# Kernel tuning notes

Measured on AMD Instinct MI355X. Metric: run time of the kernel, lower is better.

The kernel has to match this reference:

```python
import jax, jax.numpy as jnp
import numpy as np

DIM = 512
HEADS = 8
HEAD_DIM = DIM // HEADS
B, S = 2, 4096


def rope(x):
    # x: [b, s, h, d]
    half = x.shape[-1] // 2
    freqs = 10000.0 ** (-jnp.linspace(0.0, 1.0, half, endpoint=False))  # [half]
    theta = jnp.arange(x.shape[1], dtype=jnp.float32)[None, :, None, None] * freqs[None, None, None, :]
    cos, sin = jnp.cos(theta), jnp.sin(theta)
    rx, ry = x[..., :half], x[..., half:]
    return jnp.concatenate((rx * cos - ry * sin, rx * sin + ry * cos), axis=-1)


def setup_inputs() -> dict:
    key = jax.random.key(0)
    ks = jax.random.split(key, 9)
    sd_in = 1.0 / np.sqrt(DIM)
    sd_o = 1.0 / np.sqrt(DIM)
    return {
        "x": jax.random.normal(ks[0], (B, S, DIM), jnp.float32),
        "wq_k": jax.random.normal(ks[1], (DIM, HEADS, HEAD_DIM), jnp.float32) * sd_in,
        "wq_b": jnp.zeros((HEADS, HEAD_DIM), jnp.float32),
        "wk_k": jax.random.normal(ks[2], (DIM, HEADS, HEAD_DIM), jnp.float32) * sd_in,
        "wk_b": jnp.zeros((HEADS, HEAD_DIM), jnp.float32),
        "wv_k": jax.random.normal(ks[3], (DIM, HEADS, HEAD_DIM), jnp.float32) * sd_in,
        "wv_b": jnp.zeros((HEADS, HEAD_DIM), jnp.float32),
        "wo_k": jax.random.normal(ks[4], (HEADS, HEAD_DIM, DIM), jnp.float32) * sd_o,
        "wo_b": jnp.zeros((DIM,), jnp.float32),
    }


def reference(x, wq_k, wq_b, wk_k, wk_b, wv_k, wv_b, wo_k, wo_b):
    q = rope(jnp.einsum("bsd,dhk->bshk", x, wq_k) + wq_b)
    k = rope(jnp.einsum("bsd,dhk->bshk", x, wk_k) + wk_b)
    v = jnp.einsum("bsd,dhk->bshk", x, wv_k) + wv_b
    scores = jnp.einsum("bqhd,bkhd->bhqk", q, k) / (HEAD_DIM ** 0.5)
    attn = jax.nn.softmax(scores, axis=-1)
    o = jnp.einsum("bhqk,bkhd->bqhd", attn, v)
    return jnp.einsum("bqhd,hdm->bqm", o, wo_k) + wo_b
```

## Files before the change

### kernel.cpp

```cpp
#include <hip/hip_runtime.h>

typedef __bf16 bf16x4 __attribute__((ext_vector_type(4)));
typedef __bf16 bf16x8 __attribute__((ext_vector_type(8)));
typedef float  f32x4  __attribute__((ext_vector_type(4)));

#define MFMA(a, b, c) __builtin_amdgcn_mfma_f32_16x16x32_bf16(a, b, c, 0, 0, 0)

static constexpr int kHeads = 8;
static constexpr int kS     = 4096;

#define CSC 0.18033688011112042f
#define LF  (13.287712379549449f / 32.0f)
#define INV2PI 0.15915494309189535f

__device__ inline float fexp2(float x) {
#if __has_builtin(__builtin_amdgcn_exp2f)
  return __builtin_amdgcn_exp2f(x);
#else
  return __expf(x * 0.6931471805599453f);
#endif
}
__device__ inline float fsin_rev(float rev) {
#if __has_builtin(__builtin_amdgcn_sinf)
  return __builtin_amdgcn_sinf(rev);
#else
  return __sinf(rev * 6.283185307179586f);
#endif
}
__device__ inline float fcos_rev(float rev) {
#if __has_builtin(__builtin_amdgcn_cosf)
  return __builtin_amdgcn_cosf(rev);
#else
  return __cosf(rev * 6.283185307179586f);
#endif
}

__device__ inline int perm32(int d) {
  return (((d >> 2) & 3) << 3) + (((d >> 4) & 1) << 2) + (d & 3);
}

__device__ inline void gl16(const void* src, void* lds) {
  __builtin_amdgcn_global_load_lds(
      (const __attribute__((address_space(1))) unsigned int*)src,
      (__attribute__((address_space(3))) unsigned int*)lds, 16, 0, 0);
}

__global__ __launch_bounds__(256) void wprep(
    const float* __restrict__ w0, const float* __restrict__ w1,
    const float* __restrict__ w2, __bf16* __restrict__ dstb) {
  const int kb32 = blockIdx.x, m = blockIdx.y;
  const float* W = (m == 0) ? w0 : (m == 1) ? w1 : w2;
  bf16x8* dst = (bf16x8*)dstb;
  for (int e = threadIdx.x; e < 2048; e += 256) {
    int lg = e >> 9, col = e & 511;
    bf16x8 v;
    #pragma unroll
    for (int j = 0; j < 8; ++j) {
      int k = kb32 * 32 + 4 * lg + (j & 3) + 16 * (j >> 2);
      v[j] = (__bf16)W[(size_t)k * 512 + col];
    }
    dst[(((size_t)m * 16 + kb32) * 4 + lg) * 512 + col] = v;
  }
}

__global__ __launch_bounds__(256) void qkv(
    const float* __restrict__ x, const __bf16* __restrict__ Wqkvb,
    const float* __restrict__ bq, const float* __restrict__ bk,
    const float* __restrict__ bv,
    __bf16* __restrict__ Qb, __bf16* __restrict__ Kb, __bf16* __restrict__ Vt)
{
  const int tt   = blockIdx.x;
  const int hp   = blockIdx.y;
  const int wave = threadIdx.x >> 6;
  const int lane = threadIdx.x & 63;
  const int l15  = lane & 15;
  const int lg   = lane >> 4;

  const int tok0 = tt * 64 + wave * 16;
  const float* xrow = x + (size_t)(tok0 + l15) * 512;
  const bf16x8* Wf = (const bf16x8*)Wqkvb;

  f32x4 acc[6][4];
  #pragma unroll
  for (int t = 0; t < 6; ++t)
    #pragma unroll
    for (int cb = 0; cb < 4; ++cb) acc[t][cb] = f32x4{0.f, 0.f, 0.f, 0.f};

  for (int kb32 = 0; kb32 < 16; ++kb32) {
    f32x4 xa  = *(const f32x4*)(xrow + kb32 * 32 + 4 * lg);
    f32x4 xb4 = *(const f32x4*)(xrow + kb32 * 32 + 16 + 4 * lg);
    bf16x8 af;
    af[0] = (__bf16)xa.x; af[1] = (__bf16)xa.y; af[2] = (__bf16)xa.z; af[3] = (__bf16)xa.w;
    af[4] = (__bf16)xb4.x; af[5] = (__bf16)xb4.y; af[6] = (__bf16)xb4.z; af[7] = (__bf16)xb4.w;
    #pragma unroll
    for (int t = 0; t < 6; ++t) {
      const int m = t >> 1, hh = t & 1;
      const int colb = (hp * 2 + hh) * 64;
      const bf16x8* wrow = Wf + (((size_t)m * 16 + kb32) * 4 + lg) * 512 + colb + l15;
      #pragma unroll
      for (int cb = 0; cb < 4; ++cb)
        acc[t][cb] = MFMA(af, wrow[cb * 16], acc[t][cb]);
    }
  }

  const float frrev0 = fexp2(-LF * (float)l15) * INV2PI;
  const float frrev1 = fexp2(-LF * (float)(16 + l15)) * INV2PI;
  float snv[4][2], csv[4][2];
  #pragma unroll
  for (int r = 0; r < 4; ++r) {
    float sp = (float)((tok0 + 4 * lg + r) & (kS - 1));
    #pragma unroll
    for (int cb = 0; cb < 2; ++cb) {
      float rev = sp * (cb == 0 ? frrev0 : frrev1);
      rev -= floorf(rev);
      snv[r][cb] = fsin_rev(rev);
      csv[r][cb] = fcos_rev(rev);
    }
  }

  #pragma unroll
  for (int t = 0; t < 6; ++t) {
    const int m = t >> 1, hh = t & 1;
    const int h = hp * 2 + hh;
    const float* bias = (m == 0) ? bq : (m == 1) ? bk : bv;
    #pragma unroll
    for (int cb = 0; cb < 4; ++cb) {
      float bv_ = bias[h * 64 + cb * 16 + l15];
      #pragma unroll
      for (int r = 0; r < 4; ++r) acc[t][cb][r] += bv_;
    }
    if (m < 2) {
      #pragma unroll
      for (int r = 0; r < 4; ++r)
        #pragma unroll
        for (int cb = 0; cb < 2; ++cb) {
          float rx = acc[t][cb][r], ry = acc[t][cb + 2][r];
          acc[t][cb][r]     = rx * csv[r][cb] - ry * snv[r][cb];
          acc[t][cb + 2][r] = rx * snv[r][cb] + ry * csv[r][cb];
        }
      if (m == 0) {
        #pragma unroll
        for (int cb = 0; cb < 4; ++cb)
          #pragma unroll
          for (int r = 0; r < 4; ++r) acc[t][cb][r] *= CSC;
      }
    }
    #pragma unroll
    for (int r = 0; r < 4; ++r) {
      int tok = tok0 + 4 * lg + r;
      int b = tok >> 12, srow = tok & (kS - 1);
      size_t bh = (size_t)(b * kHeads + h);
      #pragma unroll
      for (int cb = 0; cb < 4; ++cb) {
        int d = cb * 16 + l15;
        __bf16 v = (__bf16)acc[t][cb][r];
        if (m < 2) {
          int slot = (d & ~31) + perm32(d & 31);
          if (m == 0) Qb[(bh * kS + srow) * 64 + slot] = v;
          else        Kb[(bh * kS + srow) * 64 + slot] = v;
        } else {
          Vt[((size_t)bh * 64 + d) * kS + (srow & ~31) + perm32(srow & 31)] = v;
        }
      }
    }
  }
}

__global__ __launch_bounds__(512) void attn(
    const __bf16* __restrict__ Qb, const __bf16* __restrict__ Kb,
    const __bf16* __restrict__ Vt, __bf16* __restrict__ Ob)
{
  __shared__ __align__(16) char smem[32768];

  const int id   = blockIdx.x;
  const int bh   = ((id & 7) << 1) | ((id >> 3) & 1);
  const int qt   = id >> 4;
  const int tid  = threadIdx.x;
  const int wave = tid >> 6;
  const int lane = tid & 63;
  const int l15  = lane & 15;
  const int lg   = lane >> 4;

  const __bf16* Qp = Qb + (size_t)bh * kS * 64;
  const char*   Kp = (const char*)(Kb + (size_t)bh * kS * 64);
  const char*   Vp = (const char*)(Vt + (size_t)bh * 64 * kS);

  const int q0 = qt * 128 + wave * 16;

  bf16x8 qf[2];
  #pragma unroll
  for (int dh = 0; dh < 2; ++dh)
    qf[dh] = *(const bf16x8*)(Qp + (size_t)(q0 + l15) * 64 + dh * 32 + 8 * lg);

  const int srow = wave * 8 + (lane >> 3);
  const int ssw  = ((lane & 7) * 16) ^ ((srow & 7) << 4);
  const char* ksrc = Kp + (size_t)srow * 128 + ssw;
  const char* vsrc = Vp + (size_t)srow * 8192 + ssw;
  const int   kdst = wave * 1024;
  const int   vdst = 8192 + wave * 1024;

  const int swz = (l15 & 7) << 4;
  const int ka0 = l15 * 128 + ((16 * lg) ^ swz);
  const int ka1 = l15 * 128 + ((64 + 16 * lg) ^ swz);
  const int va0 = 8192 + ka0;
  const int va1 = 8192 + ka1;

  f32x4 oacc[4];
  #pragma unroll
  for (int db = 0; db < 4; ++db) oacc[db] = f32x4{0.f, 0.f, 0.f, 0.f};
  float lp = 0.f;

  {
    gl16(ksrc, smem + kdst);
    gl16(vsrc, smem + vdst);
    ksrc += 8192; vsrc += 128;
  }

  int buf = 0;
  for (int it = 0; it < kS / 64; ++it) {
    __syncthreads();
    if (it + 1 < kS / 64) {
      char* sb = smem + ((buf ^ 1) << 14);
      gl16(ksrc, sb + kdst);
      gl16(vsrc, sb + vdst);
      ksrc += 8192; vsrc += 128;
    }
    const char* sb = smem + (buf << 14);

    f32x4 sa[4];
    __builtin_amdgcn_s_setprio(1);
    #pragma unroll
    for (int kh = 0; kh < 4; ++kh) {
      sa[kh] = f32x4{0.f, 0.f, 0.f, 0.f};
      bf16x8 kf0 = *(const bf16x8*)(sb + kh * 2048 + ka0);
      bf16x8 kf1 = *(const bf16x8*)(sb + kh * 2048 + ka1);
      sa[kh] = MFMA(kf0, qf[0], sa[kh]);
      sa[kh] = MFMA(kf1, qf[1], sa[kh]);
    }
    __builtin_amdgcn_s_setprio(0);

    bf16x8 pa[2];
    #pragma unroll
    for (int kh = 0; kh < 4; ++kh)
      #pragma unroll
      for (int rr = 0; rr < 4; ++rr) {
        float p = fexp2(sa[kh][rr]);
        lp += p;
        pa[kh >> 1][(kh & 1) * 4 + rr] = (__bf16)p;
      }

    __builtin_amdgcn_s_setprio(1);
    #pragma unroll
    for (int db = 0; db < 4; ++db) {
      bf16x8 vf0 = *(const bf16x8*)(sb + db * 2048 + va0);
      bf16x8 vf1 = *(const bf16x8*)(sb + db * 2048 + va1);
      oacc[db] = MFMA(vf0, pa[0], oacc[db]);
      oacc[db] = MFMA(vf1, pa[1], oacc[db]);
    }
    __builtin_amdgcn_s_setprio(0);
    buf ^= 1;
  }

  float lrun = lp;
  lrun += __shfl_xor(lrun, 16);
  lrun += __shfl_xor(lrun, 32);
  float inv = 1.0f / lrun;

  const int b = bh >> 3, h = bh & 7;
  const int q = q0 + l15;
  #pragma unroll
  for (int db = 0; db < 4; ++db) {
    bf16x4 o4;
    #pragma unroll
    for (int rr = 0; rr < 4; ++rr) o4[rr] = (__bf16)(oacc[db][rr] * inv);
    size_t e = ((size_t)(b * kS + q)) * 512 + h * 64 + (db >> 1) * 32 + 8 * lg + 4 * (db & 1);
    *(bf16x4*)(Ob + e) = o4;
  }
}

__global__ __launch_bounds__(256) void oproj(
    const __bf16* __restrict__ Ob, const __bf16* __restrict__ Wofb,
    const float* __restrict__ wob, float* __restrict__ out)
{
  const int tt   = blockIdx.x;
  const int ct   = blockIdx.y;
  const int wave = threadIdx.x >> 6;
  const int lane = threadIdx.x & 63;
  const int l15  = lane & 15;
  const int lg   = lane >> 4;

  const int tok0 = tt * 64 + wave * 16;
  const int colbase = ct * 64;
  const __bf16* orow = Ob + (size_t)(tok0 + l15) * 512;
  const bf16x8* Wf = (const bf16x8*)Wofb;

  f32x4 acc[4];
  #pragma unroll
  for (int cb = 0; cb < 4; ++cb) acc[cb] = f32x4{0.f, 0.f, 0.f, 0.f};

  for (int kb32 = 0; kb32 < 16; ++kb32) {
    bf16x8 af = *(const bf16x8*)(orow + kb32 * 32 + 8 * lg);
    const bf16x8* wrow = Wf + ((size_t)kb32 * 4 + lg) * 512 + colbase + l15;
    #pragma unroll
    for (int cb = 0; cb < 4; ++cb)
      acc[cb] = MFMA(af, wrow[cb * 16], acc[cb]);
  }

  #pragma unroll
  for (int cb = 0; cb < 4; ++cb) {
    int col = colbase + cb * 16 + l15;
    float bv_ = wob[col];
    #pragma unroll
    for (int r = 0; r < 4; ++r) {
      int tok = tok0 + 4 * lg + r;
      out[(size_t)tok * 512 + col] = acc[cb][r] + bv_;
    }
  }
}

extern "C" void kernel_launch(void* const* d_in, const int* in_sizes, int n_in,
                              void* d_out, int out_size, void* d_ws, size_t ws_size,
                              hipStream_t stream)
{
  const float* x   = (const float*)d_in[0];
  const float* wq  = (const float*)d_in[1];
  const float* bq  = (const float*)d_in[2];
  const float* wk  = (const float*)d_in[3];
  const float* bk  = (const float*)d_in[4];
  const float* wv  = (const float*)d_in[5];
  const float* bv  = (const float*)d_in[6];
  const float* wo  = (const float*)d_in[7];
  const float* wob = (const float*)d_in[8];
  float* out = (float*)d_out;

  const size_t n = (size_t)8192 * 512;
  __bf16* Qb   = (__bf16*)d_ws;
  __bf16* Kb   = Qb + n;
  __bf16* Vt   = Kb + n;
  __bf16* Ob   = Vt + n;
  __bf16* Wqkv = Ob;
  __bf16* Wof  = Qb;

  wprep<<<dim3(16, 3), 256, 0, stream>>>(wq, wk, wv, Wqkv);
  qkv<<<dim3(128, 4), 256, 0, stream>>>(x, Wqkv, bq, bk, bv, Qb, Kb, Vt);
  attn<<<512, 512, 0, stream>>>(Qb, Kb, Vt, Ob);
  wprep<<<dim3(16, 1), 256, 0, stream>>>(wo, wo, wo, Wof);
  oproj<<<dim3(128, 8), 256, 0, stream>>>(Ob, Wof, wob, out);
}
```

Measured before the change: 136.7 us.

## Double attention key tile to 128 and split QKV projection per head

The attention kernel now stages 128 keys per iteration instead of 64, using 64KB of LDS with double buffering. This halves the number of barriers and loop iterations, and each wave issues more MFMAs per sync. The V tile layout changes to 256-byte rows with a new swizzle to match. Separately, the QKV projection launches one block per head instead of per head pair, which halves the accumulator registers and doubles the grid. The cost is that x is loaded and converted twice as often, and the larger LDS footprint may lower attention occupancy.

```diff
diff --git a/kernel.cpp b/kernel.cpp
--- a/kernel.cpp
+++ b/kernel.cpp
@@ -70,7 +70,7 @@
     __bf16* __restrict__ Qb, __bf16* __restrict__ Kb, __bf16* __restrict__ Vt)
 {
   const int tt   = blockIdx.x;
-  const int hp   = blockIdx.y;
+  const int h    = blockIdx.y;
   const int wave = threadIdx.x >> 6;
   const int lane = threadIdx.x & 63;
   const int l15  = lane & 15;
@@ -79,12 +79,13 @@
   const int tok0 = tt * 64 + wave * 16;
   const float* xrow = x + (size_t)(tok0 + l15) * 512;
   const bf16x8* Wf = (const bf16x8*)Wqkvb;
-
-  f32x4 acc[6][4];
-  #pragma unroll
-  for (int t = 0; t < 6; ++t)
-    #pragma unroll
-    for (int cb = 0; cb < 4; ++cb) acc[t][cb] = f32x4{0.f, 0.f, 0.f, 0.f};
+  const int colb = h * 64;
+
+  f32x4 acc[3][4];
+  #pragma unroll
+  for (int m = 0; m < 3; ++m)
+    #pragma unroll
+    for (int cb = 0; cb < 4; ++cb) acc[m][cb] = f32x4{0.f, 0.f, 0.f, 0.f};
 
   for (int kb32 = 0; kb32 < 16; ++kb32) {
     f32x4 xa  = *(const f32x4*)(xrow + kb32 * 32 + 4 * lg);
@@ -93,13 +94,11 @@
     af[0] = (__bf16)xa.x; af[1] = (__bf16)xa.y; af[2] = (__bf16)xa.z; af[3] = (__bf16)xa.w;
     af[4] = (__bf16)xb4.x; af[5] = (__bf16)xb4.y; af[6] = (__bf16)xb4.z; af[7] = (__bf16)xb4.w;
     #pragma unroll
-    for (int t = 0; t < 6; ++t) {
-      const int m = t >> 1, hh = t & 1;
-      const int colb = (hp * 2 + hh) * 64;
+    for (int m = 0; m < 3; ++m) {
       const bf16x8* wrow = Wf + (((size_t)m * 16 + kb32) * 4 + lg) * 512 + colb + l15;
       #pragma unroll
       for (int cb = 0; cb < 4; ++cb)
-        acc[t][cb] = MFMA(af, wrow[cb * 16], acc[t][cb]);
+        acc[m][cb] = MFMA(af, wrow[cb * 16], acc[m][cb]);
     }
   }
 
@@ -119,30 +118,28 @@
   }
 
   #pragma unroll
-  for (int t = 0; t < 6; ++t) {
-    const int m = t >> 1, hh = t & 1;
-    const int h = hp * 2 + hh;
+  for (int m = 0; m < 3; ++m) {
     const float* bias = (m == 0) ? bq : (m == 1) ? bk : bv;
     #pragma unroll
     for (int cb = 0; cb < 4; ++cb) {
-      float bv_ = bias[h * 64 + cb * 16 + l15];
-      #pragma unroll
-      for (int r = 0; r < 4; ++r) acc[t][cb][r] += bv_;
+      float bv_ = bias[colb + cb * 16 + l15];
+      #pragma unroll
+      for (int r = 0; r < 4; ++r) acc[m][cb][r] += bv_;
     }
     if (m < 2) {
       #pragma unroll
       for (int r = 0; r < 4; ++r)
         #pragma unroll
         for (int cb = 0; cb < 2; ++cb) {
-          float rx = acc[t][cb][r], ry = acc[t][cb + 2][r];
-          acc[t][cb][r]     = rx * csv[r][cb] - ry * snv[r][cb];
-          acc[t][cb + 2][r] = rx * snv[r][cb] + ry * csv[r][cb];
+          float rx = acc[m][cb][r], ry = acc[m][cb + 2][r];
+          acc[m][cb][r]     = rx * csv[r][cb] - ry * snv[r][cb];
+          acc[m][cb + 2][r] = rx * snv[r][cb] + ry * csv[r][cb];
         }
       if (m == 0) {
         #pragma unroll
         for (int cb = 0; cb < 4; ++cb)
           #pragma unroll
-          for (int r = 0; r < 4; ++r) acc[t][cb][r] *= CSC;
+          for (int r = 0; r < 4; ++r) acc[m][cb][r] *= CSC;
       }
     }
     #pragma unroll
@@ -153,7 +150,7 @@
       #pragma unroll
       for (int cb = 0; cb < 4; ++cb) {
         int d = cb * 16 + l15;
-        __bf16 v = (__bf16)acc[t][cb][r];
+        __bf16 v = (__bf16)acc[m][cb][r];
         if (m < 2) {
           int slot = (d & ~31) + perm32(d & 31);
           if (m == 0) Qb[(bh * kS + srow) * 64 + slot] = v;
@@ -170,7 +167,7 @@
     const __bf16* __restrict__ Qb, const __bf16* __restrict__ Kb,
     const __bf16* __restrict__ Vt, __bf16* __restrict__ Ob)
 {
-  __shared__ __align__(16) char smem[32768];
+  __shared__ __align__(16) char smem[65536];
 
   const int id   = blockIdx.x;
   const int bh   = ((id & 7) << 1) | ((id >> 3) & 1);
@@ -192,18 +189,22 @@
   for (int dh = 0; dh < 2; ++dh)
     qf[dh] = *(const bf16x8*)(Qp + (size_t)(q0 + l15) * 64 + dh * 32 + 8 * lg);
 
-  const int srow = wave * 8 + (lane >> 3);
-  const int ssw  = ((lane & 7) * 16) ^ ((srow & 7) << 4);
-  const char* ksrc = Kp + (size_t)srow * 128 + ssw;
-  const char* vsrc = Vp + (size_t)srow * 8192 + ssw;
-  const int   kdst = wave * 1024;
-  const int   vdst = 8192 + wave * 1024;
+  const int krow = tid >> 3;
+  const int kssw = ((tid & 7) * 16) ^ ((krow & 7) << 4);
+  const char* ksrc = Kp + (size_t)krow * 128 + kssw;
+  const int vrow = tid >> 4;
+  const int vssw = ((tid & 15) * 16) ^ ((vrow & 7) << 4);
+  const char* vsrc = Vp + (size_t)vrow * 8192 + vssw;
+  const int kdst = wave * 1024;
+  const int vdst = 16384 + wave * 1024;
 
   const int swz = (l15 & 7) << 4;
   const int ka0 = l15 * 128 + ((16 * lg) ^ swz);
   const int ka1 = l15 * 128 + ((64 + 16 * lg) ^ swz);
-  const int va0 = 8192 + ka0;
-  const int va1 = 8192 + ka1;
+  int vko[4];
+  #pragma unroll
+  for (int kv = 0; kv < 4; ++kv)
+    vko[kv] = 16384 + l15 * 256 + ((kv * 64 + 16 * lg) ^ swz);
 
   f32x4 oacc[4];
   #pragma unroll
@@ -211,26 +212,26 @@
   float lp = 0.f;
 
   {
-    gl16(ksrc, smem + kdst);
-    gl16(vsrc, smem + vdst);
-    ksrc += 8192; vsrc += 128;
+    gl16(ksrc, smem + kdst);            gl16(ksrc + 8192, smem + 8192 + kdst);
+    gl16(vsrc, smem + vdst);            gl16(vsrc + 262144, smem + 8192 + vdst);
+    ksrc += 16384; vsrc += 256;
   }
 
   int buf = 0;
-  for (int it = 0; it < kS / 64; ++it) {
+  for (int it = 0; it < kS / 128; ++it) {
     __syncthreads();
-    if (it + 1 < kS / 64) {
-      char* sb = smem + ((buf ^ 1) << 14);
-      gl16(ksrc, sb + kdst);
-      gl16(vsrc, sb + vdst);
-      ksrc += 8192; vsrc += 128;
-    }
-    const char* sb = smem + (buf << 14);
-
-    f32x4 sa[4];
+    if (it + 1 < kS / 128) {
+      char* sb = smem + ((buf ^ 1) << 15);
+      gl16(ksrc, sb + kdst);            gl16(ksrc + 8192, sb + 8192 + kdst);
+      gl16(vsrc, sb + vdst);            gl16(vsrc + 262144, sb + 8192 + vdst);
+      ksrc += 16384; vsrc += 256;
+    }
+    const char* sb = smem + (buf << 15);
+
+    f32x4 sa[8];
     __builtin_amdgcn_s_setprio(1);
     #pragma unroll
-    for (int kh = 0; kh < 4; ++kh) {
+    for (int kh = 0; kh < 8; ++kh) {
       sa[kh] = f32x4{0.f, 0.f, 0.f, 0.f};
       bf16x8 kf0 = *(const bf16x8*)(sb + kh * 2048 + ka0);
       bf16x8 kf1 = *(const bf16x8*)(sb + kh * 2048 + ka1);
@@ -239,9 +240,9 @@
     }
     __builtin_amdgcn_s_setprio(0);
 
-    bf16x8 pa[2];
-    #pragma unroll
-    for (int kh = 0; kh < 4; ++kh)
+    bf16x8 pa[4];
+    #pragma unroll
+    for (int kh = 0; kh < 8; ++kh)
       #pragma unroll
       for (int rr = 0; rr < 4; ++rr) {
         float p = fexp2(sa[kh][rr]);
@@ -252,10 +253,11 @@
     __builtin_amdgcn_s_setprio(1);
     #pragma unroll
     for (int db = 0; db < 4; ++db) {
-      bf16x8 vf0 = *(const bf16x8*)(sb + db * 2048 + va0);
-      bf16x8 vf1 = *(const bf16x8*)(sb + db * 2048 + va1);
-      oacc[db] = MFMA(vf0, pa[0], oacc[db]);
-      oacc[db] = MFMA(vf1, pa[1], oacc[db]);
+      #pragma unroll
+      for (int kv = 0; kv < 4; ++kv) {
+        bf16x8 vf = *(const bf16x8*)(sb + db * 4096 + vko[kv]);
+        oacc[db] = MFMA(vf, pa[kv], oacc[db]);
+      }
     }
     __builtin_amdgcn_s_setprio(0);
     buf ^= 1;
@@ -342,7 +344,7 @@
   __bf16* Wof  = Qb;
 
   wprep<<<dim3(16, 3), 256, 0, stream>>>(wq, wk, wv, Wqkv);
-  qkv<<<dim3(128, 4), 256, 0, stream>>>(x, Wqkv, bq, bk, bv, Qb, Kb, Vt);
+  qkv<<<dim3(128, 8), 256, 0, stream>>>(x, Wqkv, bq, bk, bv, Qb, Kb, Vt);
   attn<<<512, 512, 0, stream>>>(Qb, Kb, Vt, Ob);
   wprep<<<dim3(16, 1), 256, 0, stream>>>(wo, wo, wo, Wof);
   oproj<<<dim3(128, 8), 256, 0, stream>>>(Ob, Wof, wob, out);
```

New measurement: 145.5 us. 1.06x slower.

## Software-pipeline QK and PV across tiles with triple-buffered shared memory

Applied to the files above, without the earlier changes.

Restructures the attention main loop so that each iteration computes QK^T for the current key tile while doing the PV MFMA for the previous tile's probabilities. Shared memory grows from two to three 16KB buffers so the previous tile's V stays resident while the next tile loads. The goal is to overlap the exp2/softmax VALU work with MFMA work and remove the serial dependency between score computation and the PV product. The cost is higher LDS use per block, which may reduce occupancy, plus extra registers for the carried probability fragments.

```diff
diff --git a/kernel.cpp b/kernel.cpp
--- a/kernel.cpp
+++ b/kernel.cpp
@@ -170,7 +170,7 @@
     const __bf16* __restrict__ Qb, const __bf16* __restrict__ Kb,
     const __bf16* __restrict__ Vt, __bf16* __restrict__ Ob)
 {
-  __shared__ __align__(16) char smem[32768];
+  __shared__ __align__(16) char smem[49152];
 
   const int id   = blockIdx.x;
   const int bh   = ((id & 7) << 1) | ((id >> 3) & 1);
@@ -192,8 +192,8 @@
   for (int dh = 0; dh < 2; ++dh)
     qf[dh] = *(const bf16x8*)(Qp + (size_t)(q0 + l15) * 64 + dh * 32 + 8 * lg);
 
-  const int srow = wave * 8 + (lane >> 3);
-  const int ssw  = ((lane & 7) * 16) ^ ((srow & 7) << 4);
+  const int srow = tid >> 3;
+  const int ssw  = ((tid & 7) * 16) ^ ((srow & 7) << 4);
   const char* ksrc = Kp + (size_t)srow * 128 + ssw;
   const char* vsrc = Vp + (size_t)srow * 8192 + ssw;
   const int   kdst = wave * 1024;
@@ -209,24 +209,17 @@
   #pragma unroll
   for (int db = 0; db < 4; ++db) oacc[db] = f32x4{0.f, 0.f, 0.f, 0.f};
   float lp = 0.f;
-
+  bf16x8 paP[2], paC[2];
+
+  gl16(ksrc, smem + kdst);
+  gl16(vsrc, smem + vdst);
+  ksrc += 8192; vsrc += 128;
+  __syncthreads();
+  gl16(ksrc, smem + 16384 + kdst);
+  gl16(vsrc, smem + 16384 + vdst);
+  ksrc += 8192; vsrc += 128;
   {
-    gl16(ksrc, smem + kdst);
-    gl16(vsrc, smem + vdst);
-    ksrc += 8192; vsrc += 128;
-  }
-
-  int buf = 0;
-  for (int it = 0; it < kS / 64; ++it) {
-    __syncthreads();
-    if (it + 1 < kS / 64) {
-      char* sb = smem + ((buf ^ 1) << 14);
-      gl16(ksrc, sb + kdst);
-      gl16(vsrc, sb + vdst);
-      ksrc += 8192; vsrc += 128;
-    }
-    const char* sb = smem + (buf << 14);
-
+    const char* sb = smem;
     f32x4 sa[4];
     __builtin_amdgcn_s_setprio(1);
     #pragma unroll
@@ -238,27 +231,72 @@
       sa[kh] = MFMA(kf1, qf[1], sa[kh]);
     }
     __builtin_amdgcn_s_setprio(0);
-
-    bf16x8 pa[2];
     #pragma unroll
     for (int kh = 0; kh < 4; ++kh)
       #pragma unroll
       for (int rr = 0; rr < 4; ++rr) {
         float p = fexp2(sa[kh][rr]);
         lp += p;
-        pa[kh >> 1][(kh & 1) * 4 + rr] = (__bf16)p;
+        paP[kh >> 1][(kh & 1) * 4 + rr] = (__bf16)p;
       }
-
+  }
+
+  int btP = 0, btC = 1, btN = 2;
+  for (int t = 1; t < 64; ++t) {
+    __syncthreads();
+    if (t + 1 < 64) {
+      char* sb = smem + (btN << 14);
+      gl16(ksrc, sb + kdst);
+      gl16(vsrc, sb + vdst);
+      ksrc += 8192; vsrc += 128;
+    }
+    const char* sbC = smem + (btC << 14);
+    const char* sbP = smem + (btP << 14);
+
+    f32x4 sa[4];
     __builtin_amdgcn_s_setprio(1);
     #pragma unroll
+    for (int kh = 0; kh < 4; ++kh) {
+      sa[kh] = f32x4{0.f, 0.f, 0.f, 0.f};
+      bf16x8 kf0 = *(const bf16x8*)(sbC + kh * 2048 + ka0);
+      bf16x8 kf1 = *(const bf16x8*)(sbC + kh * 2048 + ka1);
+      sa[kh] = MFMA(kf0, qf[0], sa[kh]);
+      sa[kh] = MFMA(kf1, qf[1], sa[kh]);
+    }
+    #pragma unroll
     for (int db = 0; db < 4; ++db) {
-      bf16x8 vf0 = *(const bf16x8*)(sb + db * 2048 + va0);
-      bf16x8 vf1 = *(const bf16x8*)(sb + db * 2048 + va1);
-      oacc[db] = MFMA(vf0, pa[0], oacc[db]);
-      oacc[db] = MFMA(vf1, pa[1], oacc[db]);
+      bf16x8 vf0 = *(const bf16x8*)(sbP + db * 2048 + va0);
+      bf16x8 vf1 = *(const bf16x8*)(sbP + db * 2048 + va1);
+      oacc[db] = MFMA(vf0, paP[0], oacc[db]);
+      oacc[db] = MFMA(vf1, paP[1], oacc[db]);
     }
     __builtin_amdgcn_s_setprio(0);
-    buf ^= 1;
+
+    #pragma unroll
+    for (int kh = 0; kh < 4; ++kh)
+      #pragma unroll
+      for (int rr = 0; rr < 4; ++rr) {
+        float p = fexp2(sa[kh][rr]);
+        lp += p;
+        paC[kh >> 1][(kh & 1) * 4 + rr] = (__bf16)p;
+      }
+    paP[0] = paC[0];
+    paP[1] = paC[1];
+
+    int nb = btP; btP = btC; btC = btN; btN = nb;
+  }
+
+  {
+    const char* sbP = smem + (btP << 14);
+    __builtin_amdgcn_s_setprio(1);
+    #pragma unroll
+    for (int db = 0; db < 4; ++db) {
+      bf16x8 vf0 = *(const bf16x8*)(sbP + db * 2048 + va0);
+      bf16x8 vf1 = *(const bf16x8*)(sbP + db * 2048 + va1);
+      oacc[db] = MFMA(vf0, paP[0], oacc[db]);
+      oacc[db] = MFMA(vf1, paP[1], oacc[db]);
+    }
+    __builtin_amdgcn_s_setprio(0);
   }
 
   float lrun = lp;
```

After: 136.3 us. About the same (-0.3%).
